# Kernel optimization log

Measured on AMD Instinct MI355X. Metric: run time of the kernel, lower is better.

The kernel has to match this reference:

```python
import math
import jax, jax.numpy as jnp
from jax import lax
import numpy as np

SPARSITY = 0.05
EMBEDDING_SIZE = 2048
BATCH = 32768


def setup_inputs() -> dict:
    key = jax.random.key(0)
    k0, k1, k2 = jax.random.split(key, 3)
    x = jax.random.normal(k0, (BATCH, 28, 28), dtype=jnp.float32)
    # conv: out=5, in=1, k=3, no bias (kaiming-ish scale)
    conv_w = jax.random.normal(k1, (5, 1, 3, 3), dtype=jnp.float32) * (1.0 / math.sqrt(9))
    bn_gamma = jnp.ones((5,), jnp.float32)
    bn_beta = jnp.zeros((5,), jnp.float32)
    bn_mean = jnp.zeros((5,), jnp.float32)
    bn_var = jnp.ones((5,), jnp.float32)
    # fc: [EMBEDDING_SIZE, 320], no bias
    fc_w = jax.random.normal(k2, (EMBEDDING_SIZE, 5 * 8 * 8), dtype=jnp.float32) * (1.0 / math.sqrt(320))
    return {"x": x, "conv_w": conv_w, "bn_gamma": bn_gamma, "bn_beta": bn_beta,
            "bn_mean": bn_mean, "bn_var": bn_var, "fc_w": fc_w}


def _kwta(z):
    # k-winners-take-all: top k_active entries per row -> 1, rest -> 0.
    k_active = math.ceil(SPARSITY * z.shape[1])
    topv, _ = lax.top_k(z, k_active)          # [B, k]
    thr = topv[:, -1:]                         # kth largest per row
    binary = (z >= thr).astype(z.dtype)
    # straight-through: forward = binary, backward = identity
    return z + lax.stop_gradient(binary - z)


def reference(x, conv_w, bn_gamma, bn_beta, bn_mean, bn_var, fc_w):
    h = x[:, None, :, :]  # [B,1,28,28]
    h = lax.conv_general_dilated(h, conv_w, window_strides=(1, 1), padding="VALID",
                                 dimension_numbers=("NCHW", "OIHW", "NCHW"))  # [B,5,26,26]
    inv_std = bn_gamma / jnp.sqrt(bn_var + 1e-5)
    h = (h - bn_mean[None, :, None, None]) * inv_std[None, :, None, None] + bn_beta[None, :, None, None]
    h = jnp.maximum(h, 0.0)
    # max_pool2d(kernel=3, stride=3), floor mode -> [B,5,8,8]
    h = lax.reduce_window(h, -jnp.inf, lax.max, (1, 1, 3, 3), (1, 1, 3, 3), "VALID")
    h = h.reshape(h.shape[0], -1)              # [B,320]
    z = h @ fc_w.T                             # [B,EMBEDDING_SIZE]
    return _kwta(z)
```

## Files before the change

### kernel.cpp

```cpp
#include <hip/hip_runtime.h>
#include <math.h>

#define BATCH 32768
#define EMB   2048
#define KDIM  320
#define KACT  103

#define BM 16
#define GTHREADS 1024

#define CIMG 16

__global__ __launch_bounds__(256) void transpose_w_kernel(const float* __restrict__ W,
                                                          float* __restrict__ WT) {
  __shared__ float tile[32][33];
  const int k0 = blockIdx.x * 32;
  const int n0 = blockIdx.y * 32;
  const int tx = threadIdx.x;
  const int ty = threadIdx.y;
  for (int i = ty; i < 32; i += 8)
    tile[i][tx] = W[(size_t)(n0 + i) * KDIM + k0 + tx];
  __syncthreads();
  for (int i = ty; i < 32; i += 8)
    WT[(size_t)(k0 + i) * EMB + n0 + tx] = tile[tx][i];
}

__global__ __launch_bounds__(512) void conv_pool_kernel(const float* __restrict__ x,
                                                        const float* __restrict__ cw,
                                                        const float* __restrict__ gamma,
                                                        const float* __restrict__ beta,
                                                        const float* __restrict__ mean,
                                                        const float* __restrict__ var,
                                                        float* __restrict__ Ht) {
#pragma clang fp contract(off)
  __shared__ float xs[CIMG * 784];
  __shared__ float hs[KDIM * 17];
  __shared__ float wv[45];
  __shared__ float inv_s[5], mu_s[5], be_s[5];
  const int t  = threadIdx.x;
  const int b0 = blockIdx.x * CIMG;

  {
    const float4* src = (const float4*)(x + (size_t)b0 * 784);
    float4* dst = (float4*)xs;
    for (int i = t; i < CIMG * 196; i += 512) dst[i] = src[i];
  }
  if (t < 45) wv[t] = cw[t];
  if (t < 5) {
    inv_s[t] = gamma[t] / sqrtf(var[t] + 1e-5f);
    mu_s[t] = mean[t];
    be_s[t] = beta[t];
  }
  __syncthreads();

  const int i0   = t >> 6;
  const int lane = t & 63;
  const int py = lane >> 3;
  const int px = lane & 7;

  for (int ii = 0; ii < 2; ++ii) {
    const int img = i0 * 2 + ii;
    const float* xb = xs + img * 784;

    float xr[5][5];
#pragma unroll
    for (int i = 0; i < 5; ++i)
#pragma unroll
      for (int j = 0; j < 5; ++j)
        xr[i][j] = xb[(3 * py + i) * 28 + 3 * px + j];

#pragma unroll
    for (int c = 0; c < 5; ++c) {
      float wr[9];
#pragma unroll
      for (int i = 0; i < 9; ++i) wr[i] = wv[c * 9 + i];
      const float inv = inv_s[c], mu = mu_s[c], be = be_s[c];
      float mx = -__builtin_huge_valf();
#pragma unroll
      for (int ry = 0; ry < 3; ++ry)
#pragma unroll
        for (int rx = 0; rx < 3; ++rx) {
          float s = 0.0f;
#pragma unroll
          for (int di = 0; di < 3; ++di)
#pragma unroll
            for (int dj = 0; dj < 3; ++dj)
              s = __builtin_fmaf(xr[ry + di][rx + dj], wr[di * 3 + dj], s);
          float t1 = s - mu;
          float t2 = t1 * inv;
          float t3 = t2 + be;
          mx = fmaxf(mx, t3);
        }
      hs[(c * 64 + lane) * 17 + img] = fmaxf(mx, 0.0f);
    }
  }
  __syncthreads();

  float* dst = Ht + (size_t)blockIdx.x * (KDIM * CIMG);
  for (int i = t; i < KDIM * CIMG; i += 512) {
    const int k = i >> 4;
    const int img = i & 15;
    dst[i] = hs[k * 17 + img];
  }
}

__global__ __launch_bounds__(GTHREADS, 8) void gemm_topk_kernel(const float* __restrict__ Ht,
                                                                const float* __restrict__ WT,
                                                                float* __restrict__ out) {
  __shared__ float zb[8][EMB];
  __shared__ unsigned thr_s[BM];

  const int t    = threadIdx.x;
  const int lane = t & 63;
  const int w    = t >> 6;
  const int m0   = blockIdx.x * BM;
  const int nt   = t * 2;

  float acc[BM][2];
#pragma unroll
  for (int m = 0; m < BM; ++m) {
    acc[m][0] = 0.0f;
    acc[m][1] = 0.0f;
  }

  const float* Ap = Ht + (size_t)blockIdx.x * (KDIM * BM);
  const float* wp = WT + nt;

#pragma unroll 4
  for (int k = 0; k < KDIM; ++k) {
    const float* ak = Ap + (size_t)k * BM;
    float av[BM];
#pragma unroll
    for (int m = 0; m < BM; ++m) av[m] = ak[m];
    const float2 bb = *(const float2*)(wp + (size_t)k * EMB);
#pragma unroll
    for (int m = 0; m < BM; ++m) {
      acc[m][0] = __builtin_fmaf(av[m], bb.x, acc[m][0]);
      acc[m][1] = __builtin_fmaf(av[m], bb.y, acc[m][1]);
    }
  }

#pragma unroll
  for (int m = 0; m < 8; ++m)
    *(float2*)&zb[m][nt] = *(const float2*)&acc[8 + m][0];
  __syncthreads();

  if (w >= 8) {
    const unsigned* row = (const unsigned*)&zb[w - 8][0];
    unsigned v[32];
#pragma unroll
    for (int j = 0; j < 32; ++j) {
      const unsigned x = row[j * 64 + lane];
      v[j] = x ^ (unsigned)(((int)x >> 31) | 0x80000000);
    }
    unsigned T = 0u;
    for (int b = 31; b >= 0; --b) {
      const unsigned cand = T | (1u << b);
      unsigned cnt = 0u;
#pragma unroll
      for (int j = 0; j < 32; ++j)
        cnt += (unsigned)__popcll(__ballot(v[j] >= cand));
      if (cnt >= KACT) T = cand;
    }
    if (lane == 0) thr_s[w] = T;
  }
  __syncthreads();

#pragma unroll
  for (int m = 0; m < 8; ++m) {
    const float2 p = *(const float2*)&zb[m][nt];
    const unsigned thr = thr_s[8 + m];
    unsigned ux = __float_as_uint(p.x); ux ^= (unsigned)(((int)ux >> 31) | 0x80000000);
    unsigned uy = __float_as_uint(p.y); uy ^= (unsigned)(((int)uy >> 31) | 0x80000000);
    float2 o;
    o.x = (ux >= thr) ? 1.0f : 0.0f;
    o.y = (uy >= thr) ? 1.0f : 0.0f;
    *(float2*)(out + (size_t)(m0 + 8 + m) * EMB + nt) = o;
  }
  __syncthreads();

#pragma unroll
  for (int m = 0; m < 8; ++m)
    *(float2*)&zb[m][nt] = *(const float2*)&acc[m][0];
  __syncthreads();

  if (w < 8) {
    const unsigned* row = (const unsigned*)&zb[w][0];
    unsigned v[32];
#pragma unroll
    for (int j = 0; j < 32; ++j) {
      const unsigned x = row[j * 64 + lane];
      v[j] = x ^ (unsigned)(((int)x >> 31) | 0x80000000);
    }
    unsigned T = 0u;
    for (int b = 31; b >= 0; --b) {
      const unsigned cand = T | (1u << b);
      unsigned cnt = 0u;
#pragma unroll
      for (int j = 0; j < 32; ++j)
        cnt += (unsigned)__popcll(__ballot(v[j] >= cand));
      if (cnt >= KACT) T = cand;
    }
    if (lane == 0) thr_s[w] = T;
  }
  __syncthreads();

#pragma unroll
  for (int m = 0; m < 8; ++m) {
    const float2 p = *(const float2*)&zb[m][nt];
    const unsigned thr = thr_s[m];
    unsigned ux = __float_as_uint(p.x); ux ^= (unsigned)(((int)ux >> 31) | 0x80000000);
    unsigned uy = __float_as_uint(p.y); uy ^= (unsigned)(((int)uy >> 31) | 0x80000000);
    float2 o;
    o.x = (ux >= thr) ? 1.0f : 0.0f;
    o.y = (uy >= thr) ? 1.0f : 0.0f;
    *(float2*)(out + (size_t)(m0 + m) * EMB + nt) = o;
  }
}

extern "C" void kernel_launch(void* const* d_in, const int* in_sizes, int n_in,
                              void* d_out, int out_size, void* d_ws, size_t ws_size,
                              hipStream_t stream) {
  const float* x      = (const float*)d_in[0];
  const float* conv_w = (const float*)d_in[1];
  const float* gamma  = (const float*)d_in[2];
  const float* beta   = (const float*)d_in[3];
  const float* mean   = (const float*)d_in[4];
  const float* var    = (const float*)d_in[5];
  const float* fc_w   = (const float*)d_in[6];
  float* out = (float*)d_out;

  float* Ht = (float*)d_ws;
  float* WT = (float*)d_ws + (size_t)KDIM * BATCH;

  transpose_w_kernel<<<dim3(KDIM / 32, EMB / 32), dim3(32, 8), 0, stream>>>(fc_w, WT);
  conv_pool_kernel<<<BATCH / CIMG, 512, 0, stream>>>(x, conv_w, gamma, beta, mean, var, Ht);
  gemm_topk_kernel<<<BATCH / BM, GTHREADS, 0, stream>>>(Ht, WT, out);
}
```

Before: 884.8 us.

## Fuse conv-pool into GEMM/top-k kernel and swizzle shared z buffer for vector reads

```diff
diff --git a/kernel.cpp b/kernel.cpp
--- a/kernel.cpp
+++ b/kernel.cpp
@@ -10,6 +10,8 @@
 #define GTHREADS 1024
 
 #define CIMG 16
+
+typedef unsigned uint32x4 __attribute__((ext_vector_type(4)));
 
 __global__ __launch_bounds__(256) void transpose_w_kernel(const float* __restrict__ W,
                                                           float* __restrict__ WT) {
@@ -25,25 +27,36 @@
     WT[(size_t)(k0 + i) * EMB + n0 + tx] = tile[tx][i];
 }
 
-__global__ __launch_bounds__(512) void conv_pool_kernel(const float* __restrict__ x,
-                                                        const float* __restrict__ cw,
-                                                        const float* __restrict__ gamma,
-                                                        const float* __restrict__ beta,
-                                                        const float* __restrict__ mean,
-                                                        const float* __restrict__ var,
-                                                        float* __restrict__ Ht) {
+__global__ __launch_bounds__(GTHREADS, 8) void fused_conv_gemm_topk(
+    const float* __restrict__ x,
+    const float* __restrict__ cw,
+    const float* __restrict__ gamma,
+    const float* __restrict__ beta,
+    const float* __restrict__ mean,
+    const float* __restrict__ var,
+    float* __restrict__ HtW,
+    const float* __restrict__ HtR,
+    const float* __restrict__ WT,
+    float* __restrict__ out) {
 #pragma clang fp contract(off)
-  __shared__ float xs[CIMG * 784];
-  __shared__ float hs[KDIM * 17];
+  __shared__ __attribute__((aligned(16))) float smem[18432];
   __shared__ float wv[45];
   __shared__ float inv_s[5], mu_s[5], be_s[5];
-  const int t  = threadIdx.x;
-  const int b0 = blockIdx.x * CIMG;
+  __shared__ unsigned thr_s[BM];
+
+  float* const xs = smem;
+  float* const hs = smem + 12544;
+  float* const zb = smem;
+
+  const int t    = threadIdx.x;
+  const int lane = t & 63;
+  const int w    = t >> 6;
+  const int b0   = blockIdx.x * CIMG;
 
   {
     const float4* src = (const float4*)(x + (size_t)b0 * 784);
     float4* dst = (float4*)xs;
-    for (int i = t; i < CIMG * 196; i += 512) dst[i] = src[i];
+    for (int i = t; i < CIMG * 196; i += GTHREADS) dst[i] = src[i];
   }
   if (t < 45) wv[t] = cw[t];
   if (t < 5) {
@@ -53,14 +66,11 @@
   }
   __syncthreads();
 
-  const int i0   = t >> 6;
-  const int lane = t & 63;
-  const int py = lane >> 3;
-  const int px = lane & 7;
-
-  for (int ii = 0; ii < 2; ++ii) {
-    const int img = i0 * 2 + ii;
+  {
+    const int img = w;
     const float* xb = xs + img * 784;
+    const int py = lane >> 3;
+    const int px = lane & 7;
 
     float xr[5][5];
 #pragma unroll
@@ -96,25 +106,18 @@
   }
   __syncthreads();
 
-  float* dst = Ht + (size_t)blockIdx.x * (KDIM * CIMG);
-  for (int i = t; i < KDIM * CIMG; i += 512) {
-    const int k = i >> 4;
-    const int img = i & 15;
-    dst[i] = hs[k * 17 + img];
-  }
-}
-
-__global__ __launch_bounds__(GTHREADS, 8) void gemm_topk_kernel(const float* __restrict__ Ht,
-                                                                const float* __restrict__ WT,
-                                                                float* __restrict__ out) {
-  __shared__ float zb[8][EMB];
-  __shared__ unsigned thr_s[BM];
-
-  const int t    = threadIdx.x;
-  const int lane = t & 63;
-  const int w    = t >> 6;
-  const int m0   = blockIdx.x * BM;
-  const int nt   = t * 2;
+  {
+    float* dst = HtW + (size_t)blockIdx.x * (KDIM * CIMG);
+    for (int i = t; i < KDIM * CIMG; i += GTHREADS) {
+      const int k = i >> 4;
+      const int img = i & 15;
+      dst[i] = hs[k * 17 + img];
+    }
+  }
+  __syncthreads();
+
+  const int m0 = blockIdx.x * BM;
+  const int nt = t * 2;
 
   float acc[BM][2];
 #pragma unroll
@@ -123,7 +126,7 @@
     acc[m][1] = 0.0f;
   }
 
-  const float* Ap = Ht + (size_t)blockIdx.x * (KDIM * BM);
+  const float* Ap = HtR + (size_t)blockIdx.x * (KDIM * BM);
   const float* wp = WT + nt;
 
 #pragma unroll 4
@@ -140,26 +143,41 @@
     }
   }
 
+  const int cW  = t >> 1;
+  const int cWs = cW ^ ((cW >> 3) & 7);
+  char* const zbase = (char*)zb;
+  char* const wbase = zbase + (size_t)cWs * 16 + (size_t)(t & 1) * 8;
+
 #pragma unroll
   for (int m = 0; m < 8; ++m)
-    *(float2*)&zb[m][nt] = *(const float2*)&acc[8 + m][0];
+    *(float2*)(wbase + (size_t)m * 8192) = *(const float2*)&acc[8 + m][0];
   __syncthreads();
 
   if (w >= 8) {
-    const unsigned* row = (const unsigned*)&zb[w - 8][0];
-    unsigned v[32];
-#pragma unroll
-    for (int j = 0; j < 32; ++j) {
-      const unsigned x = row[j * 64 + lane];
-      v[j] = x ^ (unsigned)(((int)x >> 31) | 0x80000000);
+    const char* rowb = zbase + (size_t)(w - 8) * 8192;
+    uint32x4 v4[8];
+#pragma unroll
+    for (int j = 0; j < 8; ++j) {
+      const int c  = (lane << 3) | j;
+      const int cs = c ^ (lane & 7);
+      uint32x4 u = *(const uint32x4*)(rowb + (size_t)cs * 16);
+#pragma unroll
+      for (int e = 0; e < 4; ++e)
+        u[e] = u[e] ^ (unsigned)(((int)u[e] >> 31) | 0x80000000);
+      v4[j] = u;
+      asm volatile("" : "+v"(v4[j]));
     }
     unsigned T = 0u;
     for (int b = 31; b >= 0; --b) {
       const unsigned cand = T | (1u << b);
       unsigned cnt = 0u;
 #pragma unroll
-      for (int j = 0; j < 32; ++j)
-        cnt += (unsigned)__popcll(__ballot(v[j] >= cand));
+      for (int j = 0; j < 8; ++j) {
+        cnt += (unsigned)__popcll(__ballot(v4[j][0] >= cand));
+        cnt += (unsigned)__popcll(__ballot(v4[j][1] >= cand));
+        cnt += (unsigned)__popcll(__ballot(v4[j][2] >= cand));
+        cnt += (unsigned)__popcll(__ballot(v4[j][3] >= cand));
+      }
       if (cnt >= KACT) T = cand;
     }
     if (lane == 0) thr_s[w] = T;
@@ -168,7 +186,7 @@
 
 #pragma unroll
   for (int m = 0; m < 8; ++m) {
-    const float2 p = *(const float2*)&zb[m][nt];
+    const float2 p = *(const float2*)(wbase + (size_t)m * 8192);
     const unsigned thr = thr_s[8 + m];
     unsigned ux = __float_as_uint(p.x); ux ^= (unsigned)(((int)ux >> 31) | 0x80000000);
     unsigned uy = __float_as_uint(p.y); uy ^= (unsigned)(((int)uy >> 31) | 0x80000000);
@@ -181,24 +199,34 @@
 
 #pragma unroll
   for (int m = 0; m < 8; ++m)
-    *(float2*)&zb[m][nt] = *(const float2*)&acc[m][0];
+    *(float2*)(wbase + (size_t)m * 8192) = *(const float2*)&acc[m][0];
   __syncthreads();
 
   if (w < 8) {
-    const unsigned* row = (const unsigned*)&zb[w][0];
-    unsigned v[32];
-#pragma unroll
-    for (int j = 0; j < 32; ++j) {
-      const unsigned x = row[j * 64 + lane];
-      v[j] = x ^ (unsigned)(((int)x >> 31) | 0x80000000);
+    const char* rowb = zbase + (size_t)w * 8192;
+    uint32x4 v4[8];
+#pragma unroll
+    for (int j = 0; j < 8; ++j) {
+      const int c  = (lane << 3) | j;
+      const int cs = c ^ (lane & 7);
+      uint32x4 u = *(const uint32x4*)(rowb + (size_t)cs * 16);
+#pragma unroll
+      for (int e = 0; e < 4; ++e)
+        u[e] = u[e] ^ (unsigned)(((int)u[e] >> 31) | 0x80000000);
+      v4[j] = u;
+      asm volatile("" : "+v"(v4[j]));
     }
     unsigned T = 0u;
     for (int b = 31; b >= 0; --b) {
       const unsigned cand = T | (1u << b);
       unsigned cnt = 0u;
 #pragma unroll
-      for (int j = 0; j < 32; ++j)
-        cnt += (unsigned)__popcll(__ballot(v[j] >= cand));
+      for (int j = 0; j < 8; ++j) {
+        cnt += (unsigned)__popcll(__ballot(v4[j][0] >= cand));
+        cnt += (unsigned)__popcll(__ballot(v4[j][1] >= cand));
+        cnt += (unsigned)__popcll(__ballot(v4[j][2] >= cand));
+        cnt += (unsigned)__popcll(__ballot(v4[j][3] >= cand));
+      }
       if (cnt >= KACT) T = cand;
     }
     if (lane == 0) thr_s[w] = T;
@@ -207,7 +235,7 @@
 
 #pragma unroll
   for (int m = 0; m < 8; ++m) {
-    const float2 p = *(const float2*)&zb[m][nt];
+    const float2 p = *(const float2*)(wbase + (size_t)m * 8192);
     const unsigned thr = thr_s[m];
     unsigned ux = __float_as_uint(p.x); ux ^= (unsigned)(((int)ux >> 31) | 0x80000000);
     unsigned uy = __float_as_uint(p.y); uy ^= (unsigned)(((int)uy >> 31) | 0x80000000);
@@ -234,6 +262,6 @@
   float* WT = (float*)d_ws + (size_t)KDIM * BATCH;
 
   transpose_w_kernel<<<dim3(KDIM / 32, EMB / 32), dim3(32, 8), 0, stream>>>(fc_w, WT);
-  conv_pool_kernel<<<BATCH / CIMG, 512, 0, stream>>>(x, conv_w, gamma, beta, mean, var, Ht);
-  gemm_topk_kernel<<<BATCH / BM, GTHREADS, 0, stream>>>(Ht, WT, out);
+  fused_conv_gemm_topk<<<BATCH / CIMG, GTHREADS, 0, stream>>>(
+      x, conv_w, gamma, beta, mean, var, Ht, Ht, WT, out);
 }
```

After: 824.0 us. 6.9% less time.
